# Optimization experiments

Hardware: AMD Instinct MI355X
Metric: run time of the kernel (lower is better)

## Reference

```python
import jax, jax.numpy as jnp
import numpy as np

HEAD_COUNT = 8  # matches init_kwargs head_count

def _branch(q_in, k_in, v_in, Wq, bq, Wk, bk, Wv, bv):
    # q_in/k_in/v_in: [B, N, D]. Linear (efficient) attention, per-head.
    B, N, D = q_in.shape
    H = HEAD_COUNT
    hd = D // H
    q = q_in @ Wq + bq            # [B, N, D]
    k = k_in @ Wk + bk
    v = v_in @ Wv + bv
    # permute(0,2,1) then contiguous channel slices per head == [B,H,hd,N]
    q = q.reshape(B, N, H, hd).transpose(0, 2, 3, 1)  # [B,H,hd,Nq]
    k = k.reshape(B, N, H, hd).transpose(0, 2, 3, 1)  # [B,H,hd,Nk]
    v = v.reshape(B, N, H, hd).transpose(0, 2, 3, 1)  # [B,H,hd,Nk]
    q = jax.nn.softmax(q, axis=3)  # softmax over sequence positions (torch dim=2)
    k = jax.nn.softmax(k, axis=2)  # softmax over head channels (torch dim=1)
    # context = k @ v^T : [B,H,hd_c,hd_d]
    ctx = jnp.einsum('bhcn,bhdn->bhcd', k, v)
    # attended = context^T @ q : [B,H,hd_d,Nq]
    att = jnp.einsum('bhcd,bhcn->bhdn', ctx, q)
    # concat heads along channel dim, then transpose -> [B, Nq, D]
    return att.reshape(B, D, N).transpose(0, 2, 1)

def setup_inputs() -> dict:
    key = jax.random.key(0)
    ks = jax.random.split(key, 16)
    B, N, D = 4, 8192, 256
    s = 0.02
    inp = {
        'f1': jax.random.normal(ks[0], (B, N, D), jnp.float32),
        'f2': jax.random.normal(ks[1], (B, N, D), jnp.float32),
        'f3': jax.random.normal(ks[2], (B, N, D), jnp.float32),
        'f4': jax.random.normal(ks[3], (B, N, D), jnp.float32),
        'f1_pos_embed': jax.random.normal(ks[4], (B, N, D), jnp.float32),
        'f2_pos_embed': jax.random.normal(ks[5], (B, N, D), jnp.float32),
        'f3_pos_embed': jax.random.normal(ks[6], (B, N, D), jnp.float32),
        'f4_pos_embed': jax.random.normal(ks[7], (B, N, D), jnp.float32),
        'Wq': jax.random.normal(ks[8], (3, D, D), jnp.float32) * s,
        'bq': jax.random.normal(ks[9], (3, D), jnp.float32) * s,
        'Wk': jax.random.normal(ks[10], (3, D, D), jnp.float32) * s,
        'bk': jax.random.normal(ks[11], (3, D), jnp.float32) * s,
        'Wv': jax.random.normal(ks[12], (3, D, D), jnp.float32) * s,
        'bv': jax.random.normal(ks[13], (3, D), jnp.float32) * s,
        'Wrp': jax.random.normal(ks[14], (3 * D, D), jnp.float32) * s,
        'brp': jax.random.normal(ks[15], (D,), jnp.float32) * s,
    }
    return inp

def reference(f1, f2, f3, f4, f1_pos_embed, f2_pos_embed, f3_pos_embed, f4_pos_embed,
              Wq, bq, Wk, bk, Wv, bv, Wrp, brp):
    q_in = f1 + f1_pos_embed
    agg21 = _branch(q_in, f2 + f2_pos_embed, f2, Wq[0], bq[0], Wk[0], bk[0], Wv[0], bv[0])
    agg31 = _branch(q_in, f3 + f3_pos_embed, f3, Wq[1], bq[1], Wk[1], bk[1], Wv[1], bv[1])
    agg41 = _branch(q_in, f4 + f4_pos_embed, f4, Wq[2], bq[2], Wk[2], bk[2], Wv[2], bv[2])
    out = jnp.concatenate([agg21, agg31, agg41], axis=-1)  # [B, N, 3D]
    return out @ Wrp + brp  # dropout p=0.0 -> identity
```

## Files before the change

kernel.cpp:

```cpp
#include <hip/hip_runtime.h>
#include <hip/hip_bf16.h>

typedef __attribute__((ext_vector_type(8))) short short8;
typedef __attribute__((ext_vector_type(4))) short shortx4;
typedef __attribute__((ext_vector_type(4))) float floatx4;
typedef __attribute__((ext_vector_type(16))) float floatx16;

#define N_SEQ 8192
#define M_ROWS 32768

__device__ __forceinline__ unsigned short f2bf(float f) {
    unsigned int x = __builtin_bit_cast(unsigned int, f);
    x += 0x7fff + ((x >> 16) & 1);
    return (unsigned short)(x >> 16);
}

__global__ __launch_bounds__(256) void transpose_w(
    const float* __restrict__ Wq, const float* __restrict__ Wk,
    const float* __restrict__ Wv, unsigned short* __restrict__ Wt)
{
    int job = blockIdx.x;
    int k = blockIdx.y;
    int n = threadIdx.x;
    const float* src =
        (job < 3) ? (Wq + job * 65536) :
        (job < 6) ? (Wk + (job - 3) * 65536) :
                    (Wv + (job - 6) * 65536);
    Wt[(size_t)job * 65536 + n * 256 + k] = f2bf(src[k * 256 + n]);
}

__global__ __launch_bounds__(512, 4) void projq_kernel(
    const float* __restrict__ f1, const float* __restrict__ p1,
    const float* __restrict__ bq, const unsigned short* __restrict__ Wt,
    unsigned short* __restrict__ expQ, float* __restrict__ S)
{
    __shared__ __align__(16) unsigned short As[64][264];
    int m0 = blockIdx.x * 64;
    int b = m0 >> 13;
    int tid = threadIdx.x;
    int lane = tid & 63, wave = tid >> 6;
    int wm = wave >> 2, wn4 = wave & 3;
    int quad = lane >> 4, l15 = lane & 15;

    {
        int srow = tid >> 3, seg = tid & 7;
        const float* fr = f1 + (size_t)(m0 + srow) * 256;
        const float* pr = p1 + (size_t)(m0 + srow) * 256;
        #pragma unroll
        for (int q = 0; q < 4; q++) {
            int c0 = q * 64 + seg * 8;
            float4 x0 = *(const float4*)(fr + c0);
            float4 x1 = *(const float4*)(fr + c0 + 4);
            float4 y0 = *(const float4*)(pr + c0);
            float4 y1 = *(const float4*)(pr + c0 + 4);
            short8 v;
            v[0] = (short)f2bf(x0.x + y0.x); v[1] = (short)f2bf(x0.y + y0.y);
            v[2] = (short)f2bf(x0.z + y0.z); v[3] = (short)f2bf(x0.w + y0.w);
            v[4] = (short)f2bf(x1.x + y1.x); v[5] = (short)f2bf(x1.y + y1.y);
            v[6] = (short)f2bf(x1.z + y1.z); v[7] = (short)f2bf(x1.w + y1.w);
            *(short8*)&As[srow][c0] = v;
        }
    }
    __syncthreads();

    for (int nj = 0; nj < 6; nj++) {
        int j = nj >> 1;
        int n0 = (nj & 1) * 128;
        const unsigned short* Wj = Wt + (size_t)j * 65536;

        floatx4 acc[2][2];
        #pragma unroll
        for (int sm = 0; sm < 2; sm++)
            #pragma unroll
            for (int sn = 0; sn < 2; sn++)
                #pragma unroll
                for (int r = 0; r < 4; r++) acc[sm][sn][r] = 0.0f;

        #pragma unroll
        for (int ks = 0; ks < 8; ks++) {
            short8 af[2], bfr[2];
            #pragma unroll
            for (int sm = 0; sm < 2; sm++)
                af[sm] = *(const short8*)&As[wm * 32 + sm * 16 + l15][ks * 32 + quad * 8];
            #pragma unroll
            for (int sn = 0; sn < 2; sn++) {
                int ncol = n0 + wn4 * 32 + sn * 16 + l15;
                bfr[sn] = *(const short8*)(Wj + (size_t)ncol * 256 + ks * 32 + quad * 8);
            }
            #pragma unroll
            for (int sm = 0; sm < 2; sm++)
                #pragma unroll
                for (int sn = 0; sn < 2; sn++)
                    acc[sm][sn] = __builtin_amdgcn_mfma_f32_16x16x32_bf16(
                        af[sm], bfr[sn], acc[sm][sn], 0, 0, 0);
        }

        float colsum[2] = {0.f, 0.f};
        #pragma unroll
        for (int sm = 0; sm < 2; sm++)
            #pragma unroll
            for (int sn = 0; sn < 2; sn++) {
                float bb = bq[j * 256 + n0 + wn4 * 32 + sn * 16 + l15];
                #pragma unroll
                for (int r = 0; r < 4; r++) {
                    float e = __expf(acc[sm][sn][r] + bb);
                    colsum[sn] += e;
                    int row = m0 + wm * 32 + sm * 16 + quad * 4 + r;
                    int col = j * 256 + n0 + wn4 * 32 + sn * 16 + l15;
                    expQ[(size_t)row * 768 + col] = f2bf(e);
                }
            }
        #pragma unroll
        for (int sn = 0; sn < 2; sn++) {
            float v = colsum[sn];
            v += __shfl_xor(v, 16, 64);
            v += __shfl_xor(v, 32, 64);
            if (quad == 0)
                atomicAdd(&S[b * 768 + j * 256 + n0 + wn4 * 32 + sn * 16 + l15], v);
        }
    }
}

__global__ __launch_bounds__(512, 4) void projkv_ctx(
    const float* __restrict__ f2, const float* __restrict__ f3, const float* __restrict__ f4,
    const float* __restrict__ p2, const float* __restrict__ p3, const float* __restrict__ p4,
    const float* __restrict__ bk, const float* __restrict__ bv,
    const unsigned short* __restrict__ Wt, float* __restrict__ ctx)
{
    __shared__ __align__(16) unsigned short sh[36864];

    int tid = threadIdx.x;
    int lane = tid & 63, wn = tid >> 6;
    int quad = lane >> 4, l15 = lane & 15;
    int srow = tid >> 3, seg = tid & 7;

    int gbase = -1;
    int cur_ib = -1;
    const float *fin = nullptr, *pin = nullptr;
    const unsigned short *Wk_ = nullptr, *Wv_ = nullptr;
    float bkk[2] = {0.f, 0.f}, bvv[2] = {0.f, 0.f};
    floatx16 ctxacc;

    for (int j = 0; j < 3; j++) {
        int tau = blockIdx.x * 3 + j;
        int ib = tau >> 7;
        if (ib != cur_ib) {
            if (gbase >= 0) {
                int d = lane & 31;
                #pragma unroll
                for (int reg = 0; reg < 16; reg++) {
                    int cc = (reg & 3) + 8 * (reg >> 2) + 4 * (lane >> 5);
                    atomicAdd(&ctx[(size_t)gbase * 1024 + cc * 32 + d], ctxacc[reg]);
                }
            }
            cur_ib = ib;
            int b = ib & 3, i = ib >> 2;
            fin = ((i == 0) ? f2 : (i == 1) ? f3 : f4) + (size_t)b * N_SEQ * 256;
            pin = ((i == 0) ? p2 : (i == 1) ? p3 : p4) + (size_t)b * N_SEQ * 256;
            Wk_ = Wt + (size_t)(3 + i) * 65536;
            Wv_ = Wt + (size_t)(6 + i) * 65536;
            #pragma unroll
            for (int sn = 0; sn < 2; sn++) {
                bkk[sn] = bk[i * 256 + wn * 32 + sn * 16 + l15];
                bvv[sn] = bv[i * 256 + wn * 32 + sn * 16 + l15];
            }
            gbase = i * 32 + b * 8 + wn;
            #pragma unroll
            for (int q = 0; q < 16; q++) ctxacc[q] = 0.0f;
        }
        int m0 = (tau & 127) * 64;

        __syncthreads();
        {
            const float* fr = fin + (size_t)(m0 + srow) * 256;
            const float* pr = pin + (size_t)(m0 + srow) * 256;
            #pragma unroll
            for (int q = 0; q < 4; q++) {
                int c0 = q * 64 + seg * 8;
                float4 x0 = *(const float4*)(fr + c0);
                float4 x1 = *(const float4*)(fr + c0 + 4);
                float4 y0 = *(const float4*)(pr + c0);
                float4 y1 = *(const float4*)(pr + c0 + 4);
                short8 vv, kk;
                vv[0] = (short)f2bf(x0.x); kk[0] = (short)f2bf(x0.x + y0.x);
                vv[1] = (short)f2bf(x0.y); kk[1] = (short)f2bf(x0.y + y0.y);
                vv[2] = (short)f2bf(x0.z); kk[2] = (short)f2bf(x0.z + y0.z);
                vv[3] = (short)f2bf(x0.w); kk[3] = (short)f2bf(x0.w + y0.w);
                vv[4] = (short)f2bf(x1.x); kk[4] = (short)f2bf(x1.x + y1.x);
                vv[5] = (short)f2bf(x1.y); kk[5] = (short)f2bf(x1.y + y1.y);
                vv[6] = (short)f2bf(x1.z); kk[6] = (short)f2bf(x1.z + y1.z);
                vv[7] = (short)f2bf(x1.w); kk[7] = (short)f2bf(x1.w + y1.w);
                *(short8*)&sh[srow * 264 + c0] = kk;
                *(short8*)&sh[18432 + srow * 264 + c0] = vv;
            }
        }
        __syncthreads();

        floatx4 acc[4][2];
        #pragma unroll
        for (int sm = 0; sm < 4; sm++)
            #pragma unroll
            for (int sn = 0; sn < 2; sn++)
                #pragma unroll
                for (int r = 0; r < 4; r++) acc[sm][sn][r] = 0.0f;
        #pragma unroll
        for (int ks = 0; ks < 8; ks++) {
            short8 af[4], bfr[2];
            #pragma unroll
            for (int sm = 0; sm < 4; sm++)
                af[sm] = *(const short8*)&sh[(sm * 16 + l15) * 264 + ks * 32 + quad * 8];
            #pragma unroll
            for (int sn = 0; sn < 2; sn++) {
                int ncol = wn * 32 + sn * 16 + l15;
                bfr[sn] = *(const short8*)(Wk_ + (size_t)ncol * 256 + ks * 32 + quad * 8);
            }
            #pragma unroll
            for (int sm = 0; sm < 4; sm++)
                #pragma unroll
                for (int sn = 0; sn < 2; sn++)
                    acc[sm][sn] = __builtin_amdgcn_mfma_f32_16x16x32_bf16(
                        af[sm], bfr[sn], acc[sm][sn], 0, 0, 0);
        }
        #pragma unroll
        for (int sm = 0; sm < 4; sm++)
            #pragma unroll
            for (int r = 0; r < 4; r++) {
                float e0 = __expf(acc[sm][0][r] + bkk[0]);
                float e1 = __expf(acc[sm][1][r] + bkk[1]);
                float t = e0 + e1;
                t += __shfl_xor(t, 1, 64);
                t += __shfl_xor(t, 2, 64);
                t += __shfl_xor(t, 4, 64);
                t += __shfl_xor(t, 8, 64);
                float inv = 1.0f / t;
                acc[sm][0][r] = e0 * inv;
                acc[sm][1][r] = e1 * inv;
            }
        __syncthreads();
        #pragma unroll
        for (int sm = 0; sm < 4; sm++)
            #pragma unroll
            for (int sn = 0; sn < 2; sn++) {
                shortx4 v;
                #pragma unroll
                for (int r = 0; r < 4; r++) v[r] = (short)f2bf(acc[sm][sn][r]);
                *(shortx4*)&sh[(wn * 32 + sn * 16 + l15) * 72 + sm * 16 + quad * 4] = v;
            }

        #pragma unroll
        for (int sm = 0; sm < 4; sm++)
            #pragma unroll
            for (int sn = 0; sn < 2; sn++)
                #pragma unroll
                for (int r = 0; r < 4; r++) acc[sm][sn][r] = 0.0f;
        #pragma unroll
        for (int ks = 0; ks < 8; ks++) {
            short8 af[4], bfr[2];
            #pragma unroll
            for (int sm = 0; sm < 4; sm++)
                af[sm] = *(const short8*)&sh[18432 + (sm * 16 + l15) * 264 + ks * 32 + quad * 8];
            #pragma unroll
            for (int sn = 0; sn < 2; sn++) {
                int ncol = wn * 32 + sn * 16 + l15;
                bfr[sn] = *(const short8*)(Wv_ + (size_t)ncol * 256 + ks * 32 + quad * 8);
            }
            #pragma unroll
            for (int sm = 0; sm < 4; sm++)
                #pragma unroll
                for (int sn = 0; sn < 2; sn++)
                    acc[sm][sn] = __builtin_amdgcn_mfma_f32_16x16x32_bf16(
                        af[sm], bfr[sn], acc[sm][sn], 0, 0, 0);
        }
        __syncthreads();
        #pragma unroll
        for (int sm = 0; sm < 4; sm++)
            #pragma unroll
            for (int sn = 0; sn < 2; sn++) {
                shortx4 v;
                #pragma unroll
                for (int r = 0; r < 4; r++) v[r] = (short)f2bf(acc[sm][sn][r] + bvv[sn]);
                *(shortx4*)&sh[18432 + (wn * 32 + sn * 16 + l15) * 72 + sm * 16 + quad * 4] = v;
            }

        {
            int hc = wn * 32 + (lane & 31);
            int nb = (lane >> 5) * 8;
            #pragma unroll
            for (int s = 0; s < 4; s++) {
                short8 afr  = *(const short8*)&sh[hc * 72 + s * 16 + nb];
                short8 bfr2 = *(const short8*)&sh[18432 + hc * 72 + s * 16 + nb];
                ctxacc = __builtin_amdgcn_mfma_f32_32x32x16_bf16(afr, bfr2, ctxacc, 0, 0, 0);
            }
        }
    }

    if (gbase >= 0) {
        int d = lane & 31;
        #pragma unroll
        for (int reg = 0; reg < 16; reg++) {
            int cc = (reg & 3) + 8 * (reg >> 2) + 4 * (lane >> 5);
            atomicAdd(&ctx[(size_t)gbase * 1024 + cc * 32 + d], ctxacc[reg]);
        }
    }
}

__global__ __launch_bounds__(256) void wtilde_kernel(
    const float* __restrict__ ctx, const float* __restrict__ S,
    const float* __restrict__ Wrp, unsigned short* __restrict__ Wtld)
{
    __shared__ float cp[1024];
    int g = blockIdx.x;
    int i = g >> 5, b = (g >> 3) & 3, h = g & 7;
    int t = threadIdx.x;
    #pragma unroll
    for (int q = 0; q < 4; q++) {
        int idx = t + q * 256;
        int c = idx >> 5;
        cp[idx] = ctx[(size_t)g * 1024 + idx] / S[b * 768 + i * 256 + h * 32 + c];
    }
    __syncthreads();
    float accv[32];
    #pragma unroll
    for (int c = 0; c < 32; c++) accv[c] = 0.0f;
    for (int d = 0; d < 32; d++) {
        float w = Wrp[(size_t)(i * 256 + h * 32 + d) * 256 + t];
        #pragma unroll
        for (int c = 0; c < 32; c++) accv[c] += cp[c * 32 + d] * w;
    }
    for (int c = 0; c < 32; c++)
        Wtld[((size_t)b * 256 + t) * 768 + i * 256 + h * 32 + c] = f2bf(accv[c]);
}

__global__ __launch_bounds__(512, 4) void out_kernel(
    const unsigned short* __restrict__ expQ, const unsigned short* __restrict__ Wtld,
    const float* __restrict__ brp, float* __restrict__ outp)
{
    __shared__ __align__(16) unsigned short As[64][72];
    int m0 = blockIdx.x * 64;
    int b = m0 >> 13;
    const unsigned short* Wb = Wtld + (size_t)b * 256 * 768;
    int tid = threadIdx.x;
    int lane = tid & 63, wave = tid >> 6;
    int wm = wave >> 2, wn = wave & 3;
    int quad = lane >> 4, l15 = lane & 15;
    int srow = tid >> 3, skc = (tid & 7) * 8;

    floatx4 acc[2][4];
    #pragma unroll
    for (int sm = 0; sm < 2; sm++)
        #pragma unroll
        for (int sn = 0; sn < 4; sn++)
            #pragma unroll
            for (int r = 0; r < 4; r++) acc[sm][sn][r] = 0.0f;

    for (int kt = 0; kt < 12; kt++) {
        __syncthreads();
        *(short8*)&As[srow][skc] =
            *(const short8*)(expQ + (size_t)(m0 + srow) * 768 + kt * 64 + skc);
        __syncthreads();
        #pragma unroll
        for (int kc = 0; kc < 64; kc += 32) {
            short8 af[2], bfr[4];
            #pragma unroll
            for (int sm = 0; sm < 2; sm++)
                af[sm] = *(const short8*)&As[wm * 32 + sm * 16 + l15][kc + quad * 8];
            #pragma unroll
            for (int sn = 0; sn < 4; sn++) {
                int ncol = wn * 64 + sn * 16 + l15;
                bfr[sn] = *(const short8*)(Wb + (size_t)ncol * 768 + kt * 64 + kc + quad * 8);
            }
            #pragma unroll
            for (int sm = 0; sm < 2; sm++)
                #pragma unroll
                for (int sn = 0; sn < 4; sn++)
                    acc[sm][sn] = __builtin_amdgcn_mfma_f32_16x16x32_bf16(
                        af[sm], bfr[sn], acc[sm][sn], 0, 0, 0);
        }
    }

    float bb[4];
    #pragma unroll
    for (int sn = 0; sn < 4; sn++) bb[sn] = brp[wn * 64 + sn * 16 + l15];
    #pragma unroll
    for (int sm = 0; sm < 2; sm++)
        #pragma unroll
        for (int sn = 0; sn < 4; sn++)
            #pragma unroll
            for (int r = 0; r < 4; r++) {
                int row = m0 + wm * 32 + sm * 16 + quad * 4 + r;
                int col = wn * 64 + sn * 16 + l15;
                outp[(size_t)row * 256 + col] = acc[sm][sn][r] + bb[sn];
            }
}

extern "C" void kernel_launch(void* const* d_in, const int* in_sizes, int n_in,
                              void* d_out, int out_size, void* d_ws, size_t ws_size,
                              hipStream_t stream)
{
    (void)in_sizes; (void)n_in; (void)out_size; (void)ws_size;
    const float* f1  = (const float*)d_in[0];
    const float* f2  = (const float*)d_in[1];
    const float* f3  = (const float*)d_in[2];
    const float* f4  = (const float*)d_in[3];
    const float* p1  = (const float*)d_in[4];
    const float* p2  = (const float*)d_in[5];
    const float* p3  = (const float*)d_in[6];
    const float* p4  = (const float*)d_in[7];
    const float* Wq  = (const float*)d_in[8];
    const float* bq  = (const float*)d_in[9];
    const float* Wk  = (const float*)d_in[10];
    const float* bk  = (const float*)d_in[11];
    const float* Wv  = (const float*)d_in[12];
    const float* bv  = (const float*)d_in[13];
    const float* Wrp = (const float*)d_in[14];
    const float* brp = (const float*)d_in[15];

    char* ws = (char*)d_ws;
    unsigned short* expQ = (unsigned short*)(ws);
    unsigned short* Wt   = (unsigned short*)(ws + 50331648);
    unsigned short* Wtld = (unsigned short*)(ws + 51511296);
    float*          ctx  = (float*)(ws + 53084160);
    float*          S    = (float*)(ws + 53477376);

    hipMemsetAsync(ctx, 0, 393216 + 12288, stream);

    transpose_w<<<dim3(9, 256), 256, 0, stream>>>(Wq, Wk, Wv, Wt);
    projq_kernel<<<dim3(512), 512, 0, stream>>>(f1, p1, bq, Wt, expQ, S);
    projkv_ctx<<<dim3(512), 512, 0, stream>>>(f2, f3, f4, p2, p3, p4, bk, bv, Wt, ctx);
    wtilde_kernel<<<dim3(96), 256, 0, stream>>>(ctx, S, Wrp, Wtld);
    out_kernel<<<dim3(512), 512, 0, stream>>>(expQ, Wtld, brp, (float*)d_out);
}
```

Before: 445.4 us.

## Halve row tiles to double grid size and add shared-memory tiled weight transpose

The projection, context and output kernels now process 32 rows per block instead of 64, so the grids double to 1024 blocks. Launch bounds rise to 8 waves per SIMD and shared-memory footprints shrink, with padded strides adjusted and 8-byte split loads for the narrower context staging. The weight transpose moves from one element per thread to 64x64 tiles staged through LDS with vectorized reads and writes. The goal is better occupancy and load balance across CUs. The cost is that each weight tile is reused over fewer rows, raising global/L2 traffic for weights, and more atomic adds hit S and ctx.

Result: slower. 546.8 us (+22.8%).

```diff
diff --git a/kernel.cpp b/kernel.cpp
--- a/kernel.cpp
+++ b/kernel.cpp
@@ -15,57 +15,91 @@
     return (unsigned short)(x >> 16);
 }
 
+__device__ __forceinline__ short8 ld_b64x2(const unsigned short* p) {
+    shortx4 a = *(const shortx4*)p;
+    shortx4 b = *(const shortx4*)(p + 4);
+    short8 r;
+    r[0] = a[0]; r[1] = a[1]; r[2] = a[2]; r[3] = a[3];
+    r[4] = b[0]; r[5] = b[1]; r[6] = b[2]; r[7] = b[3];
+    return r;
+}
+
 __global__ __launch_bounds__(256) void transpose_w(
     const float* __restrict__ Wq, const float* __restrict__ Wk,
     const float* __restrict__ Wv, unsigned short* __restrict__ Wt)
 {
+    __shared__ unsigned short tile[64][72];
     int job = blockIdx.x;
-    int k = blockIdx.y;
-    int n = threadIdx.x;
+    int tt = blockIdx.y;
+    int k0 = (tt >> 2) * 64, n0 = (tt & 3) * 64;
     const float* src =
         (job < 3) ? (Wq + job * 65536) :
         (job < 6) ? (Wk + (job - 3) * 65536) :
                     (Wv + (job - 6) * 65536);
-    Wt[(size_t)job * 65536 + n * 256 + k] = f2bf(src[k * 256 + n]);
-}
-
-__global__ __launch_bounds__(512, 4) void projq_kernel(
+    int tid = threadIdx.x;
+    {
+        int r = tid >> 2, cs = (tid & 3) * 16;
+        const float* s = src + (size_t)(k0 + r) * 256 + n0 + cs;
+        #pragma unroll
+        for (int h = 0; h < 2; h++) {
+            float4 x0 = *(const float4*)(s + h * 8);
+            float4 x1 = *(const float4*)(s + h * 8 + 4);
+            short8 v;
+            v[0] = (short)f2bf(x0.x); v[1] = (short)f2bf(x0.y);
+            v[2] = (short)f2bf(x0.z); v[3] = (short)f2bf(x0.w);
+            v[4] = (short)f2bf(x1.x); v[5] = (short)f2bf(x1.y);
+            v[6] = (short)f2bf(x1.z); v[7] = (short)f2bf(x1.w);
+            *(short8*)&tile[r][cs + h * 8] = v;
+        }
+    }
+    __syncthreads();
+    {
+        int rn = tid >> 2, ks = (tid & 3) * 16;
+        unsigned short tmp[16];
+        #pragma unroll
+        for (int q = 0; q < 16; q++) tmp[q] = tile[ks + q][rn];
+        short8 v0, v1;
+        #pragma unroll
+        for (int q = 0; q < 8; q++) { v0[q] = (short)tmp[q]; v1[q] = (short)tmp[q + 8]; }
+        unsigned short* dst = Wt + (size_t)job * 65536 + (size_t)(n0 + rn) * 256 + k0 + ks;
+        *(short8*)dst = v0;
+        *(short8*)(dst + 8) = v1;
+    }
+}
+
+__global__ __launch_bounds__(512, 8) void projq_kernel(
     const float* __restrict__ f1, const float* __restrict__ p1,
     const float* __restrict__ bq, const unsigned short* __restrict__ Wt,
     unsigned short* __restrict__ expQ, float* __restrict__ S)
 {
-    __shared__ __align__(16) unsigned short As[64][264];
-    int m0 = blockIdx.x * 64;
+    __shared__ __align__(16) unsigned short As[32][264];
+    int m0 = blockIdx.x * 32;
     int b = m0 >> 13;
     int tid = threadIdx.x;
     int lane = tid & 63, wave = tid >> 6;
-    int wm = wave >> 2, wn4 = wave & 3;
     int quad = lane >> 4, l15 = lane & 15;
 
     {
-        int srow = tid >> 3, seg = tid & 7;
-        const float* fr = f1 + (size_t)(m0 + srow) * 256;
-        const float* pr = p1 + (size_t)(m0 + srow) * 256;
-        #pragma unroll
-        for (int q = 0; q < 4; q++) {
-            int c0 = q * 64 + seg * 8;
-            float4 x0 = *(const float4*)(fr + c0);
-            float4 x1 = *(const float4*)(fr + c0 + 4);
-            float4 y0 = *(const float4*)(pr + c0);
-            float4 y1 = *(const float4*)(pr + c0 + 4);
+        int srow = tid >> 4, seg = tid & 15;
+        const float* fr = f1 + (size_t)(m0 + srow) * 256 + seg * 16;
+        const float* pr = p1 + (size_t)(m0 + srow) * 256 + seg * 16;
+        #pragma unroll
+        for (int h = 0; h < 2; h++) {
+            float4 x0 = *(const float4*)(fr + h * 8);
+            float4 x1 = *(const float4*)(fr + h * 8 + 4);
+            float4 y0 = *(const float4*)(pr + h * 8);
+            float4 y1 = *(const float4*)(pr + h * 8 + 4);
             short8 v;
             v[0] = (short)f2bf(x0.x + y0.x); v[1] = (short)f2bf(x0.y + y0.y);
             v[2] = (short)f2bf(x0.z + y0.z); v[3] = (short)f2bf(x0.w + y0.w);
             v[4] = (short)f2bf(x1.x + y1.x); v[5] = (short)f2bf(x1.y + y1.y);
             v[6] = (short)f2bf(x1.z + y1.z); v[7] = (short)f2bf(x1.w + y1.w);
-            *(short8*)&As[srow][c0] = v;
+            *(short8*)&As[srow][seg * 16 + h * 8] = v;
         }
     }
     __syncthreads();
 
-    for (int nj = 0; nj < 6; nj++) {
-        int j = nj >> 1;
-        int n0 = (nj & 1) * 128;
+    for (int j = 0; j < 3; j++) {
         const unsigned short* Wj = Wt + (size_t)j * 65536;
 
         floatx4 acc[2][2];
@@ -81,10 +115,10 @@
             short8 af[2], bfr[2];
             #pragma unroll
             for (int sm = 0; sm < 2; sm++)
-                af[sm] = *(const short8*)&As[wm * 32 + sm * 16 + l15][ks * 32 + quad * 8];
-            #pragma unroll
-            for (int sn = 0; sn < 2; sn++) {
-                int ncol = n0 + wn4 * 32 + sn * 16 + l15;
+                af[sm] = *(const short8*)&As[sm * 16 + l15][ks * 32 + quad * 8];
+            #pragma unroll
+            for (int sn = 0; sn < 2; sn++) {
+                int ncol = wave * 32 + sn * 16 + l15;
                 bfr[sn] = *(const short8*)(Wj + (size_t)ncol * 256 + ks * 32 + quad * 8);
             }
             #pragma unroll
@@ -100,13 +134,13 @@
         for (int sm = 0; sm < 2; sm++)
             #pragma unroll
             for (int sn = 0; sn < 2; sn++) {
-                float bb = bq[j * 256 + n0 + wn4 * 32 + sn * 16 + l15];
+                float bb = bq[j * 256 + wave * 32 + sn * 16 + l15];
                 #pragma unroll
                 for (int r = 0; r < 4; r++) {
                     float e = __expf(acc[sm][sn][r] + bb);
                     colsum[sn] += e;
-                    int row = m0 + wm * 32 + sm * 16 + quad * 4 + r;
-                    int col = j * 256 + n0 + wn4 * 32 + sn * 16 + l15;
+                    int row = m0 + sm * 16 + quad * 4 + r;
+                    int col = j * 256 + wave * 32 + sn * 16 + l15;
                     expQ[(size_t)row * 768 + col] = f2bf(e);
                 }
             }
@@ -116,23 +150,26 @@
             v += __shfl_xor(v, 16, 64);
             v += __shfl_xor(v, 32, 64);
             if (quad == 0)
-                atomicAdd(&S[b * 768 + j * 256 + n0 + wn4 * 32 + sn * 16 + l15], v);
-        }
-    }
-}
-
-__global__ __launch_bounds__(512, 4) void projkv_ctx(
+                atomicAdd(&S[b * 768 + j * 256 + wave * 32 + sn * 16 + l15], v);
+        }
+    }
+}
+
+#define KV_RS 296
+#define KV_R1 9472
+#define KV_PS 36
+__global__ __launch_bounds__(512, 8) void projkv_ctx(
     const float* __restrict__ f2, const float* __restrict__ f3, const float* __restrict__ f4,
     const float* __restrict__ p2, const float* __restrict__ p3, const float* __restrict__ p4,
     const float* __restrict__ bk, const float* __restrict__ bv,
     const unsigned short* __restrict__ Wt, float* __restrict__ ctx)
 {
-    __shared__ __align__(16) unsigned short sh[36864];
+    __shared__ __align__(16) unsigned short sh[18944];
 
     int tid = threadIdx.x;
     int lane = tid & 63, wn = tid >> 6;
     int quad = lane >> 4, l15 = lane & 15;
-    int srow = tid >> 3, seg = tid & 7;
+    int srow = tid >> 4, seg = tid & 15;
 
     int gbase = -1;
     int cur_ib = -1;
@@ -143,7 +180,7 @@
 
     for (int j = 0; j < 3; j++) {
         int tau = blockIdx.x * 3 + j;
-        int ib = tau >> 7;
+        int ib = tau >> 8;
         if (ib != cur_ib) {
             if (gbase >= 0) {
                 int d = lane & 31;
@@ -168,19 +205,18 @@
             #pragma unroll
             for (int q = 0; q < 16; q++) ctxacc[q] = 0.0f;
         }
-        int m0 = (tau & 127) * 64;
+        int m0 = (tau & 255) * 32;
 
         __syncthreads();
         {
-            const float* fr = fin + (size_t)(m0 + srow) * 256;
-            const float* pr = pin + (size_t)(m0 + srow) * 256;
-            #pragma unroll
-            for (int q = 0; q < 4; q++) {
-                int c0 = q * 64 + seg * 8;
-                float4 x0 = *(const float4*)(fr + c0);
-                float4 x1 = *(const float4*)(fr + c0 + 4);
-                float4 y0 = *(const float4*)(pr + c0);
-                float4 y1 = *(const float4*)(pr + c0 + 4);
+            const float* fr = fin + (size_t)(m0 + srow) * 256 + seg * 16;
+            const float* pr = pin + (size_t)(m0 + srow) * 256 + seg * 16;
+            #pragma unroll
+            for (int h = 0; h < 2; h++) {
+                float4 x0 = *(const float4*)(fr + h * 8);
+                float4 x1 = *(const float4*)(fr + h * 8 + 4);
+                float4 y0 = *(const float4*)(pr + h * 8);
+                float4 y1 = *(const float4*)(pr + h * 8 + 4);
                 short8 vv, kk;
                 vv[0] = (short)f2bf(x0.x); kk[0] = (short)f2bf(x0.x + y0.x);
                 vv[1] = (short)f2bf(x0.y); kk[1] = (short)f2bf(x0.y + y0.y);
@@ -190,39 +226,39 @@
                 vv[5] = (short)f2bf(x1.y); kk[5] = (short)f2bf(x1.y + y1.y);
                 vv[6] = (short)f2bf(x1.z); kk[6] = (short)f2bf(x1.z + y1.z);
                 vv[7] = (short)f2bf(x1.w); kk[7] = (short)f2bf(x1.w + y1.w);
-                *(short8*)&sh[srow * 264 + c0] = kk;
-                *(short8*)&sh[18432 + srow * 264 + c0] = vv;
-            }
-        }
-        __syncthreads();
-
-        floatx4 acc[4][2];
-        #pragma unroll
-        for (int sm = 0; sm < 4; sm++)
+                *(short8*)&sh[srow * KV_RS + seg * 16 + h * 8] = kk;
+                *(short8*)&sh[KV_R1 + srow * KV_RS + seg * 16 + h * 8] = vv;
+            }
+        }
+        __syncthreads();
+
+        floatx4 acc[2][2];
+        #pragma unroll
+        for (int sm = 0; sm < 2; sm++)
             #pragma unroll
             for (int sn = 0; sn < 2; sn++)
                 #pragma unroll
                 for (int r = 0; r < 4; r++) acc[sm][sn][r] = 0.0f;
         #pragma unroll
         for (int ks = 0; ks < 8; ks++) {
-            short8 af[4], bfr[2];
-            #pragma unroll
-            for (int sm = 0; sm < 4; sm++)
-                af[sm] = *(const short8*)&sh[(sm * 16 + l15) * 264 + ks * 32 + quad * 8];
+            short8 af[2], bfr[2];
+            #pragma unroll
+            for (int sm = 0; sm < 2; sm++)
+                af[sm] = *(const short8*)&sh[(sm * 16 + l15) * KV_RS + ks * 32 + quad * 8];
             #pragma unroll
             for (int sn = 0; sn < 2; sn++) {
                 int ncol = wn * 32 + sn * 16 + l15;
                 bfr[sn] = *(const short8*)(Wk_ + (size_t)ncol * 256 + ks * 32 + quad * 8);
             }
             #pragma unroll
-            for (int sm = 0; sm < 4; sm++)
+            for (int sm = 0; sm < 2; sm++)
                 #pragma unroll
                 for (int sn = 0; sn < 2; sn++)
                     acc[sm][sn] = __builtin_amdgcn_mfma_f32_16x16x32_bf16(
                         af[sm], bfr[sn], acc[sm][sn], 0, 0, 0);
         }
         #pragma unroll
-        for (int sm = 0; sm < 4; sm++)
+        for (int sm = 0; sm < 2; sm++)
             #pragma unroll
             for (int r = 0; r < 4; r++) {
                 float e0 = __expf(acc[sm][0][r] + bkk[0]);
@@ -238,34 +274,34 @@
             }
         __syncthreads();
         #pragma unroll
-        for (int sm = 0; sm < 4; sm++)
+        for (int sm = 0; sm < 2; sm++)
             #pragma unroll
             for (int sn = 0; sn < 2; sn++) {
                 shortx4 v;
                 #pragma unroll
                 for (int r = 0; r < 4; r++) v[r] = (short)f2bf(acc[sm][sn][r]);
-                *(shortx4*)&sh[(wn * 32 + sn * 16 + l15) * 72 + sm * 16 + quad * 4] = v;
-            }
-
-        #pragma unroll
-        for (int sm = 0; sm < 4; sm++)
+                *(shortx4*)&sh[(wn * 32 + sn * 16 + l15) * KV_PS + sm * 16 + quad * 4] = v;
+            }
+
+        #pragma unroll
+        for (int sm = 0; sm < 2; sm++)
             #pragma unroll
             for (int sn = 0; sn < 2; sn++)
                 #pragma unroll
                 for (int r = 0; r < 4; r++) acc[sm][sn][r] = 0.0f;
         #pragma unroll
         for (int ks = 0; ks < 8; ks++) {
-            short8 af[4], bfr[2];
-            #pragma unroll
-            for (int sm = 0; sm < 4; sm++)
-                af[sm] = *(const short8*)&sh[18432 + (sm * 16 + l15) * 264 + ks * 32 + quad * 8];
+            short8 af[2], bfr[2];
+            #pragma unroll
+            for (int sm = 0; sm < 2; sm++)
+                af[sm] = *(const short8*)&sh[KV_R1 + (sm * 16 + l15) * KV_RS + ks * 32 + quad * 8];
             #pragma unroll
             for (int sn = 0; sn < 2; sn++) {
                 int ncol = wn * 32 + sn * 16 + l15;
                 bfr[sn] = *(const short8*)(Wv_ + (size_t)ncol * 256 + ks * 32 + quad * 8);
             }
             #pragma unroll
-            for (int sm = 0; sm < 4; sm++)
+            for (int sm = 0; sm < 2; sm++)
                 #pragma unroll
                 for (int sn = 0; sn < 2; sn++)
                     acc[sm][sn] = __builtin_amdgcn_mfma_f32_16x16x32_bf16(
@@ -273,22 +309,22 @@
         }
         __syncthreads();
         #pragma unroll
-        for (int sm = 0; sm < 4; sm++)
+        for (int sm = 0; sm < 2; sm++)
             #pragma unroll
             for (int sn = 0; sn < 2; sn++) {
                 shortx4 v;
                 #pragma unroll
                 for (int r = 0; r < 4; r++) v[r] = (short)f2bf(acc[sm][sn][r] + bvv[sn]);
-                *(shortx4*)&sh[18432 + (wn * 32 + sn * 16 + l15) * 72 + sm * 16 + quad * 4] = v;
+                *(shortx4*)&sh[KV_R1 + (wn * 32 + sn * 16 + l15) * KV_PS + sm * 16 + quad * 4] = v;
             }
 
         {
             int hc = wn * 32 + (lane & 31);
             int nb = (lane >> 5) * 8;
             #pragma unroll
-            for (int s = 0; s < 4; s++) {
-                short8 afr  = *(const short8*)&sh[hc * 72 + s * 16 + nb];
-                short8 bfr2 = *(const short8*)&sh[18432 + hc * 72 + s * 16 + nb];
+            for (int s = 0; s < 2; s++) {
+                short8 afr  = ld_b64x2(&sh[hc * KV_PS + s * 16 + nb]);
+                short8 bfr2 = ld_b64x2(&sh[KV_R1 + hc * KV_PS + s * 16 + nb]);
                 ctxacc = __builtin_amdgcn_mfma_f32_32x32x16_bf16(afr, bfr2, ctxacc, 0, 0, 0);
             }
         }
@@ -331,64 +367,63 @@
         Wtld[((size_t)b * 256 + t) * 768 + i * 256 + h * 32 + c] = f2bf(accv[c]);
 }
 
-__global__ __launch_bounds__(512, 4) void out_kernel(
+__global__ __launch_bounds__(512, 8) void out_kernel(
     const unsigned short* __restrict__ expQ, const unsigned short* __restrict__ Wtld,
     const float* __restrict__ brp, float* __restrict__ outp)
 {
-    __shared__ __align__(16) unsigned short As[64][72];
-    int m0 = blockIdx.x * 64;
+    __shared__ __align__(16) unsigned short As[32][72];
+    int m0 = blockIdx.x * 32;
     int b = m0 >> 13;
     const unsigned short* Wb = Wtld + (size_t)b * 256 * 768;
     int tid = threadIdx.x;
     int lane = tid & 63, wave = tid >> 6;
-    int wm = wave >> 2, wn = wave & 3;
     int quad = lane >> 4, l15 = lane & 15;
-    int srow = tid >> 3, skc = (tid & 7) * 8;
-
-    floatx4 acc[2][4];
+    int srow = tid >> 4, k4 = (tid & 15) * 4;
+
+    floatx4 acc[2][2];
     #pragma unroll
     for (int sm = 0; sm < 2; sm++)
         #pragma unroll
-        for (int sn = 0; sn < 4; sn++)
+        for (int sn = 0; sn < 2; sn++)
             #pragma unroll
             for (int r = 0; r < 4; r++) acc[sm][sn][r] = 0.0f;
 
     for (int kt = 0; kt < 12; kt++) {
         __syncthreads();
-        *(short8*)&As[srow][skc] =
-            *(const short8*)(expQ + (size_t)(m0 + srow) * 768 + kt * 64 + skc);
+        *(shortx4*)&As[srow][k4] =
+            *(const shortx4*)(expQ + (size_t)(m0 + srow) * 768 + kt * 64 + k4);
         __syncthreads();
         #pragma unroll
         for (int kc = 0; kc < 64; kc += 32) {
-            short8 af[2], bfr[4];
-            #pragma unroll
-            for (int sm = 0; sm < 2; sm++)
-                af[sm] = *(const short8*)&As[wm * 32 + sm * 16 + l15][kc + quad * 8];
-            #pragma unroll
-            for (int sn = 0; sn < 4; sn++) {
-                int ncol = wn * 64 + sn * 16 + l15;
+            short8 af[2], bfr[2];
+            #pragma unroll
+            for (int sm = 0; sm < 2; sm++)
+                af[sm] = *(const short8*)&As[sm * 16 + l15][kc + quad * 8];
+            #pragma unroll
+            for (int sn = 0; sn < 2; sn++) {
+                int ncol = wave * 32 + sn * 16 + l15;
                 bfr[sn] = *(const short8*)(Wb + (size_t)ncol * 768 + kt * 64 + kc + quad * 8);
             }
             #pragma unroll
             for (int sm = 0; sm < 2; sm++)
                 #pragma unroll
-                for (int sn = 0; sn < 4; sn++)
+                for (int sn = 0; sn < 2; sn++)
                     acc[sm][sn] = __builtin_amdgcn_mfma_f32_16x16x32_bf16(
                         af[sm], bfr[sn], acc[sm][sn], 0, 0, 0);
         }
     }
 
-    float bb[4];
+    float bb[2];
     #pragma unroll
-    for (int sn = 0; sn < 4; sn++) bb[sn] = brp[wn * 64 + sn * 16 + l15];
+    for (int sn = 0; sn < 2; sn++) bb[sn] = brp[wave * 32 + sn * 16 + l15];
     #pragma unroll
     for (int sm = 0; sm < 2; sm++)
         #pragma unroll
-        for (int sn = 0; sn < 4; sn++)
+        for (int sn = 0; sn < 2; sn++)
             #pragma unroll
             for (int r = 0; r < 4; r++) {
-                int row = m0 + wm * 32 + sm * 16 + quad * 4 + r;
-                int col = wn * 64 + sn * 16 + l15;
+                int row = m0 + sm * 16 + quad * 4 + r;
+                int col = wave * 32 + sn * 16 + l15;
                 outp[(size_t)row * 256 + col] = acc[sm][sn][r] + bb[sn];
             }
 }
@@ -424,9 +459,9 @@
 
     hipMemsetAsync(ctx, 0, 393216 + 12288, stream);
 
-    transpose_w<<<dim3(9, 256), 256, 0, stream>>>(Wq, Wk, Wv, Wt);
-    projq_kernel<<<dim3(512), 512, 0, stream>>>(f1, p1, bq, Wt, expQ, S);
-    projkv_ctx<<<dim3(512), 512, 0, stream>>>(f2, f3, f4, p2, p3, p4, bk, bv, Wt, ctx);
+    transpose_w<<<dim3(9, 16), 256, 0, stream>>>(Wq, Wk, Wv, Wt);
+    projq_kernel<<<dim3(1024), 512, 0, stream>>>(f1, p1, bq, Wt, expQ, S);
+    projkv_ctx<<<dim3(1024), 512, 0, stream>>>(f2, f3, f4, p2, p3, p4, bk, bv, Wt, ctx);
     wtilde_kernel<<<dim3(96), 256, 0, stream>>>(ctx, S, Wrp, Wtld);
-    out_kernel<<<dim3(512), 512, 0, stream>>>(expQ, Wtld, brp, (float*)d_out);
-}
+    out_kernel<<<dim3(1024), 512, 0, stream>>>(expQ, Wtld, brp, (float*)d_out);
+}
```
